# Performance work log

Measured on AMD Instinct MI355X. Metric: run time of the kernel, lower is better.

## Reference

```python
import jax, jax.numpy as jnp
import numpy as np

N_LAYER, D_MODEL, N_HEAD, D_HEAD, D_INNER = 4, 1024, 16, 64, 4096
QLEN, MLEN, BATCH, VOCAB = 512, 512, 4, 32000


def _layer_norm(x, g, b, eps=1e-5):
    mu = jnp.mean(x, axis=-1, keepdims=True)
    var = jnp.mean((x - mu) ** 2, axis=-1, keepdims=True)
    return (x - mu) * jax.lax.rsqrt(var + eps) * g + b


def _rel_shift(x):
    # x: [q, k, b, n] -- TransfoXL relative shift
    q, k, b, n = x.shape
    x = jnp.pad(x, ((0, 0), (1, 0), (0, 0), (0, 0)))
    return x.reshape(k + 1, q, b, n)[1:].reshape(q, k, b, n)


def _pos_emb(klen, d):
    inv_freq = 1.0 / (10000.0 ** (jnp.arange(0, d, 2, dtype=jnp.float32) / d))
    pos = jnp.arange(klen - 1, -1, -1, dtype=jnp.float32)
    sinusoid = pos[:, None] * inv_freq[None, :]
    return jnp.concatenate([jnp.sin(sinusoid), jnp.cos(sinusoid)], axis=-1)  # [klen, d]


def setup_inputs() -> dict:
    key = jax.random.key(0)
    ks = jax.random.split(key, 12)
    s = 0.02
    rn = lambda k, shape: jax.random.normal(k, shape, jnp.float32) * s
    return {
        "token_ids": jax.random.randint(ks[0], (BATCH, QLEN), 0, VOCAB),
        "mems": rn(ks[1], (N_LAYER, MLEN, BATCH, D_MODEL)),
        "word_emb": rn(ks[2], (VOCAB, D_MODEL)),
        "qkv_w": rn(ks[3], (N_LAYER, 3 * N_HEAD * D_HEAD, D_MODEL)),
        "o_w": rn(ks[4], (N_LAYER, D_MODEL, N_HEAD * D_HEAD)),
        "r_w": rn(ks[5], (N_LAYER, N_HEAD * D_HEAD, D_MODEL)),
        "r_w_bias": rn(ks[6], (N_LAYER, N_HEAD, D_HEAD)),
        "r_r_bias": rn(ks[7], (N_LAYER, N_HEAD, D_HEAD)),
        "ln1_g": jnp.ones((N_LAYER, D_MODEL)),
        "ln1_b": jnp.zeros((N_LAYER, D_MODEL)),
        "ff_w1": rn(ks[8], (N_LAYER, D_INNER, D_MODEL)),
        "ff_b1": jnp.zeros((N_LAYER, D_INNER)),
        "ff_w2": rn(ks[9], (N_LAYER, D_MODEL, D_INNER)),
        "ff_b2": jnp.zeros((N_LAYER, D_MODEL)),
        "ln2_g": jnp.ones((N_LAYER, D_MODEL)),
        "ln2_b": jnp.zeros((N_LAYER, D_MODEL)),
    }


def reference(token_ids, mems, word_emb, qkv_w, o_w, r_w, r_w_bias, r_r_bias,
              ln1_g, ln1_b, ff_w1, ff_b1, ff_w2, ff_b2, ln2_g, ln2_b):
    B, Q = token_ids.shape
    M = mems.shape[1]
    K = M + Q
    d_model = word_emb.shape[1]
    n_head, d_head = r_w_bias.shape[1], r_w_bias.shape[2]
    nd = n_head * d_head
    scale = 1.0 / (d_head ** 0.5)

    h = word_emb[token_ids].transpose(1, 0, 2)  # [Q, B, D] (TransfoXL is time-major)
    pe = _pos_emb(K, d_model)                   # [K, D]
    # causal mask: query i may attend keys j <= i + M
    mask = jnp.arange(K)[None, :] > (jnp.arange(Q)[:, None] + M)  # [Q, K]

    for l in range(mems.shape[0]):
        cat = jnp.concatenate([mems[l], h], axis=0)          # [K, B, D]
        qkv = jnp.einsum('kbd,ed->kbe', cat, qkv_w[l])       # [K, B, 3*nd]
        q = qkv[-Q:, :, :nd].reshape(Q, B, n_head, d_head)
        k = qkv[:, :, nd:2 * nd].reshape(K, B, n_head, d_head)
        v = qkv[:, :, 2 * nd:].reshape(K, B, n_head, d_head)
        r = (pe @ r_w[l].T).reshape(K, n_head, d_head)       # [K, n, d]

        AC = jnp.einsum('ibnd,jbnd->ijbn', q + r_w_bias[l], k)
        BD = _rel_shift(jnp.einsum('ibnd,jnd->ijbn', q + r_r_bias[l], r))
        score = (AC + BD) * scale                            # [Q, K, B, n]
        score = jnp.where(mask[:, :, None, None], -1e30, score)
        prob = jax.nn.softmax(score, axis=1)
        vec = jnp.einsum('ijbn,jbnd->ibnd', prob, v).reshape(Q, B, nd)
        h = _layer_norm(h + vec @ o_w[l].T, ln1_g[l], ln1_b[l])
        ff = jax.nn.relu(h @ ff_w1[l].T + ff_b1[l]) @ ff_w2[l].T + ff_b2[l]
        h = _layer_norm(h + ff, ln2_g[l], ln2_b[l])

    return h.transpose(1, 0, 2)  # [B, Q, D] last hidden state
```

## Files before the change

kernel.cpp:

```cpp
#include <hip/hip_runtime.h>
#include <cstdint>

#define NLAYER 4
#define DMODEL 1024
#define NHEAD 16
#define DHEAD 64
#define DINNER 4096
#define QLEN 512
#define MLEN 512
#define KLEN (QLEN + MLEN)
#define BATCH 4
#define ND (NHEAD * DHEAD)

typedef unsigned short u16;
typedef __attribute__((ext_vector_type(8))) short short8;
typedef __attribute__((ext_vector_type(4))) float f32x4;
typedef __attribute__((address_space(1))) const unsigned int guint;
typedef __attribute__((address_space(3))) unsigned int luint;

__device__ __forceinline__ u16 f2b(float x) {
  unsigned u = __builtin_bit_cast(unsigned, x);
  return (u16)((u + 0x7fffu + ((u >> 16) & 1u)) >> 16);
}
__device__ __forceinline__ float b2f(u16 h) {
  return __builtin_bit_cast(float, (unsigned)h << 16);
}

__global__ __launch_bounds__(256) void conv_bf16(
    const float* __restrict__ s, u16* __restrict__ d, int n8)
{
  const int i = blockIdx.x * 256 + threadIdx.x;
  if (i >= n8) return;
  const float4 a = ((const float4*)s)[2 * i], b = ((const float4*)s)[2 * i + 1];
  union { u16 u[8]; float4 v; } p;
  p.u[0] = f2b(a.x); p.u[1] = f2b(a.y); p.u[2] = f2b(a.z); p.u[3] = f2b(a.w);
  p.u[4] = f2b(b.x); p.u[5] = f2b(b.y); p.u[6] = f2b(b.z); p.u[7] = f2b(b.w);
  ((float4*)d)[i] = p.v;
}

__global__ __launch_bounds__(256) void embed_kernel(
    const int* __restrict__ tok, const float* __restrict__ emb,
    float* __restrict__ h, u16* __restrict__ hb)
{
  const int q = blockIdx.x, b = blockIdx.y, t = threadIdx.x;
  const int id = tok[b * QLEN + q];
  const float4 v = ((const float4*)(emb + (size_t)id * DMODEL))[t];
  const size_t row = (size_t)q * BATCH + b;
  ((float4*)(h + row * DMODEL))[t] = v;
  union { u16 u[4]; float2 f; } p;
  p.u[0] = f2b(v.x); p.u[1] = f2b(v.y); p.u[2] = f2b(v.z); p.u[3] = f2b(v.w);
  *(float2*)(hb + row * DMODEL + t * 4) = p.f;
}

__global__ __launch_bounds__(256) void posemb_kernel(u16* __restrict__ pe)
{
  const int k = blockIdx.x, t = threadIdx.x;
  const float pos = (float)(KLEN - 1 - k);
  for (int i = t; i < DMODEL / 2; i += 256) {
    const float inv_freq = powf(10000.0f, -(float)(2 * i) / (float)DMODEL);
    const float a = pos * inv_freq;
    pe[(size_t)k * DMODEL + i] = f2b(sinf(a));
    pe[(size_t)k * DMODEL + DMODEL / 2 + i] = f2b(cosf(a));
  }
}

template<int OUTBF, int RELU, int BIAS>
__global__ __launch_bounds__(256) void mgemm4(
    const u16* __restrict__ A0, const u16* __restrict__ A1, int splitRow,
    const u16* __restrict__ B, void* __restrict__ Cp,
    const float* __restrict__ bias, int Kd, long sa, long sb, long sc)
{
  constexpr int MF = 4;
  constexpr int BM = 128;
  constexpr int NGA = 16;
  constexpr int GPW = 8;
  __shared__ u16 As[2][BM][64];
  __shared__ u16 Bs[2][128][64];
  const int nwg = gridDim.x * gridDim.y;
  int wg = blockIdx.y * gridDim.x + blockIdx.x;
  wg = (wg & 7) * (nwg >> 3) + (wg >> 3);
  const int bm = (wg % gridDim.x) * BM;
  const int bn = (wg / gridDim.x) * 128;
  const int t = threadIdx.x, wave = t >> 6, lane = t & 63;
  const int wm = (wave >> 1) * (MF * 16), wn = (wave & 1) * 64;
  const int lrow = lane & 15, lk = lane >> 4;
  const int gsw = ((lane & 7) ^ (lane >> 3)) * 8;
  const u16* gptr[GPW];
  int row8[GPW];
  bool isA[GPW];
#pragma unroll
  for (int c = 0; c < GPW; ++c) {
    const int g = wave * GPW + c;
    isA[c] = g < NGA;
    row8[c] = (isA[c] ? g : g - NGA) * 8;
    const int row = row8[c] + (lane >> 3);
    if (isA[c]) {
      const int ga = bm + row;
      gptr[c] = ((A1 != nullptr && ga >= splitRow)
                     ? A1 + (size_t)(ga - splitRow) * sa
                     : A0 + (size_t)ga * sa) + gsw;
    } else {
      gptr[c] = B + (size_t)(bn + row) * sb + gsw;
    }
  }
  auto STAGE = [&](int buf, int k0) {
#pragma unroll
    for (int c = 0; c < GPW; ++c) {
      luint* dst = isA[c] ? (luint*)&As[buf][row8[c]][0] : (luint*)&Bs[buf][row8[c]][0];
      __builtin_amdgcn_global_load_lds((guint*)(gptr[c] + k0), dst, 16, 0, 0);
    }
  };
  f32x4 acc[MF][4] = {};
  const int nt = Kd >> 6;
  STAGE(0, 0);
  for (int ti = 0; ti < nt; ++ti) {
    const int cur = ti & 1;
    if (ti + 1 < nt) {
      STAGE(cur ^ 1, (ti + 1) << 6);
      asm volatile("s_waitcnt vmcnt(8)" ::: "memory");
    } else {
      asm volatile("s_waitcnt vmcnt(0)" ::: "memory");
    }
    __builtin_amdgcn_s_barrier();
    __builtin_amdgcn_sched_barrier(0);
    __builtin_amdgcn_s_setprio(1);
#pragma unroll
    for (int ks = 0; ks < 2; ++ks) {
      short8 af[MF], bf[4];
#pragma unroll
      for (int x = 0; x < MF; ++x) {
        const int ra = wm + x * 16 + lrow;
        af[x] = *(const short8*)((const u16*)&As[cur][0][0] + ra * 64 + (((ks * 4 + lk) ^ (ra & 7)) * 8));
      }
#pragma unroll
      for (int x = 0; x < 4; ++x) {
        const int rb = wn + x * 16 + lrow;
        bf[x] = *(const short8*)((const u16*)&Bs[cur][0][0] + rb * 64 + (((ks * 4 + lk) ^ (rb & 7)) * 8));
      }
#pragma unroll
      for (int mi = 0; mi < MF; ++mi)
#pragma unroll
        for (int ni = 0; ni < 4; ++ni)
          acc[mi][ni] = __builtin_amdgcn_mfma_f32_16x16x32_bf16(af[mi], bf[ni], acc[mi][ni], 0, 0, 0);
    }
    __builtin_amdgcn_s_setprio(0);
    asm volatile("s_waitcnt lgkmcnt(0)" ::: "memory");
    __builtin_amdgcn_s_barrier();
    __builtin_amdgcn_sched_barrier(0);
  }
  const size_t row0 = bm + wm + lk * 4;
  const size_t col0 = bn + wn + lrow;
#pragma unroll
  for (int mi = 0; mi < MF; ++mi)
#pragma unroll
    for (int r = 0; r < 4; ++r) {
      const size_t row = row0 + mi * 16 + r;
#pragma unroll
      for (int ni = 0; ni < 4; ++ni) {
        float v = acc[mi][ni][r];
        if (BIAS) v += bias[col0 + ni * 16];
        if (RELU) v = fmaxf(v, 0.0f);
        if (OUTBF) ((u16*)Cp)[row * sc + col0 + ni * 16] = f2b(v);
        else       ((float*)Cp)[row * sc + col0 + ni * 16] = v;
      }
    }
}

template<int BIAS>
__global__ __launch_bounds__(256) void mgemm4k(
    const u16* __restrict__ A, const u16* __restrict__ B,
    float* __restrict__ C0, float* __restrict__ C1,
    const float* __restrict__ bias, int KdH, long sa, long sb, long sc)
{
  constexpr int MF = 2;
  constexpr int BM = 64;
  constexpr int NGA = 8;
  constexpr int GPW = 6;
  __shared__ u16 As[2][BM][64];
  __shared__ u16 Bs[2][128][64];
  const int z = blockIdx.z;
  A += (size_t)z * KdH;
  B += (size_t)z * KdH;
  float* C = z ? C1 : C0;
  const int nwg = gridDim.x * gridDim.y;
  int wg = blockIdx.y * gridDim.x + blockIdx.x;
  wg = (wg & 7) * (nwg >> 3) + (wg >> 3);
  const int bm = (wg % gridDim.x) * BM;
  const int bn = (wg / gridDim.x) * 128;
  const int t = threadIdx.x, wave = t >> 6, lane = t & 63;
  const int wm = (wave >> 1) * (MF * 16), wn = (wave & 1) * 64;
  const int lrow = lane & 15, lk = lane >> 4;
  const int gsw = ((lane & 7) ^ (lane >> 3)) * 8;
  const u16* gptr[GPW];
  int row8[GPW];
  bool isA[GPW];
#pragma unroll
  for (int c = 0; c < GPW; ++c) {
    const int g = wave * GPW + c;
    isA[c] = g < NGA;
    row8[c] = (isA[c] ? g : g - NGA) * 8;
    const int row = row8[c] + (lane >> 3);
    gptr[c] = isA[c] ? A + (size_t)(bm + row) * sa + gsw
                     : B + (size_t)(bn + row) * sb + gsw;
  }
  auto STAGE = [&](int buf, int k0) {
#pragma unroll
    for (int c = 0; c < GPW; ++c) {
      luint* dst = isA[c] ? (luint*)&As[buf][row8[c]][0] : (luint*)&Bs[buf][row8[c]][0];
      __builtin_amdgcn_global_load_lds((guint*)(gptr[c] + k0), dst, 16, 0, 0);
    }
  };
  f32x4 acc[MF][4] = {};
  const int nt = KdH >> 6;
  STAGE(0, 0);
  for (int ti = 0; ti < nt; ++ti) {
    const int cur = ti & 1;
    if (ti + 1 < nt) {
      STAGE(cur ^ 1, (ti + 1) << 6);
      asm volatile("s_waitcnt vmcnt(6)" ::: "memory");
    } else {
      asm volatile("s_waitcnt vmcnt(0)" ::: "memory");
    }
    __builtin_amdgcn_s_barrier();
    __builtin_amdgcn_sched_barrier(0);
    __builtin_amdgcn_s_setprio(1);
#pragma unroll
    for (int ks = 0; ks < 2; ++ks) {
      short8 af[MF], bf[4];
#pragma unroll
      for (int x = 0; x < MF; ++x) {
        const int ra = wm + x * 16 + lrow;
        af[x] = *(const short8*)((const u16*)&As[cur][0][0] + ra * 64 + (((ks * 4 + lk) ^ (ra & 7)) * 8));
      }
#pragma unroll
      for (int x = 0; x < 4; ++x) {
        const int rb = wn + x * 16 + lrow;
        bf[x] = *(const short8*)((const u16*)&Bs[cur][0][0] + rb * 64 + (((ks * 4 + lk) ^ (rb & 7)) * 8));
      }
#pragma unroll
      for (int mi = 0; mi < MF; ++mi)
#pragma unroll
        for (int ni = 0; ni < 4; ++ni)
          acc[mi][ni] = __builtin_amdgcn_mfma_f32_16x16x32_bf16(af[mi], bf[ni], acc[mi][ni], 0, 0, 0);
    }
    __builtin_amdgcn_s_setprio(0);
    asm volatile("s_waitcnt lgkmcnt(0)" ::: "memory");
    __builtin_amdgcn_s_barrier();
    __builtin_amdgcn_sched_barrier(0);
  }
  const size_t row0 = bm + wm + lk * 4;
  const size_t col0 = bn + wn + lrow;
#pragma unroll
  for (int mi = 0; mi < MF; ++mi)
#pragma unroll
    for (int r = 0; r < 4; ++r) {
      const size_t row = row0 + mi * 16 + r;
#pragma unroll
      for (int ni = 0; ni < 4; ++ni) {
        float v = acc[mi][ni][r];
        if (BIAS && z == 0) v += bias[col0 + ni * 16];
        C[row * sc + col0 + ni * 16] = v;
      }
    }
}

template<int MF, int OUTBF, int RELU, int BIAS>
__global__ __launch_bounds__(256) void mgemm3(
    const u16* __restrict__ A0, const u16* __restrict__ A1, int splitRow,
    const u16* __restrict__ B, void* __restrict__ Cp,
    const float* __restrict__ bias, int Kd, long sa, long sb, long sc,
    long bzs, long czs)
{
  constexpr int BM = MF * 32;
  constexpr int NGA = BM / 8;
  constexpr int GPW = (NGA + 16) / 4;
  __shared__ u16 As[2][BM][64];
  __shared__ u16 Bs[2][128][64];
  const int zz = blockIdx.z;
  B += (size_t)zz * bzs;
  const int nwg = gridDim.x * gridDim.y;
  int wg = blockIdx.y * gridDim.x + blockIdx.x;
  wg = (wg & 7) * (nwg >> 3) + (wg >> 3);
  const int bm = (wg % gridDim.x) * BM;
  const int bn = (wg / gridDim.x) * 128;
  const int t = threadIdx.x, wave = t >> 6, lane = t & 63;
  const int wm = (wave >> 1) * (MF * 16), wn = (wave & 1) * 64;
  const int lrow = lane & 15, lk = lane >> 4;
  const int gsw = ((lane & 7) ^ (lane >> 3)) * 8;
  const u16* gptr[GPW];
  int row8[GPW];
  bool isA[GPW];
#pragma unroll
  for (int c = 0; c < GPW; ++c) {
    const int g = wave * GPW + c;
    isA[c] = g < NGA;
    row8[c] = (isA[c] ? g : g - NGA) * 8;
    const int row = row8[c] + (lane >> 3);
    if (isA[c]) {
      const int ga = bm + row;
      gptr[c] = ((A1 != nullptr && ga >= splitRow)
                     ? A1 + (size_t)(ga - splitRow) * sa
                     : A0 + (size_t)ga * sa) + gsw;
    } else {
      gptr[c] = B + (size_t)(bn + row) * sb + gsw;
    }
  }
  auto STAGE = [&](int buf, int k0) {
#pragma unroll
    for (int c = 0; c < GPW; ++c) {
      luint* dst = isA[c] ? (luint*)&As[buf][row8[c]][0] : (luint*)&Bs[buf][row8[c]][0];
      __builtin_amdgcn_global_load_lds((guint*)(gptr[c] + k0), dst, 16, 0, 0);
    }
  };
  f32x4 acc[MF][4] = {};
  const int nt = Kd >> 6;
  STAGE(0, 0);
  __syncthreads();
  for (int ti = 0; ti < nt; ++ti) {
    const int cur = ti & 1;
    if (ti + 1 < nt) STAGE(cur ^ 1, (ti + 1) << 6);
#pragma unroll
    for (int ks = 0; ks < 2; ++ks) {
      short8 af[MF], bf[4];
#pragma unroll
      for (int x = 0; x < MF; ++x) {
        const int ra = wm + x * 16 + lrow;
        af[x] = *(const short8*)((const u16*)&As[cur][0][0] + ra * 64 + (((ks * 4 + lk) ^ (ra & 7)) * 8));
      }
#pragma unroll
      for (int x = 0; x < 4; ++x) {
        const int rb = wn + x * 16 + lrow;
        bf[x] = *(const short8*)((const u16*)&Bs[cur][0][0] + rb * 64 + (((ks * 4 + lk) ^ (rb & 7)) * 8));
      }
#pragma unroll
      for (int mi = 0; mi < MF; ++mi)
#pragma unroll
        for (int ni = 0; ni < 4; ++ni)
          acc[mi][ni] = __builtin_amdgcn_mfma_f32_16x16x32_bf16(af[mi], bf[ni], acc[mi][ni], 0, 0, 0);
    }
    __syncthreads();
  }
  const size_t row0 = bm + wm + lk * 4;
  const size_t col0 = bn + wn + lrow;
#pragma unroll
  for (int mi = 0; mi < MF; ++mi)
#pragma unroll
    for (int r = 0; r < 4; ++r) {
      const size_t row = row0 + mi * 16 + r;
#pragma unroll
      for (int ni = 0; ni < 4; ++ni) {
        float v = acc[mi][ni][r];
        if (BIAS) v += bias[col0 + ni * 16];
        if (RELU) v = fmaxf(v, 0.0f);
        if (OUTBF) ((u16*)Cp + (size_t)zz * czs)[row * sc + col0 + ni * 16] = f2b(v);
        else       ((float*)Cp + (size_t)zz * czs)[row * sc + col0 + ni * 16] = v;
      }
    }
}

__global__ __launch_bounds__(256) void bd_gemm(
    const u16* __restrict__ qkvb, const u16* __restrict__ B,
    const float* __restrict__ rrb, u16* __restrict__ S)
{
  __shared__ u16 As[128][40];
  __shared__ u16 Bs[128][40];
  const int bm = blockIdx.x * 128, bn = blockIdx.y * 128;
  if (bm + bn < 257) return;
  const int z = blockIdx.z, zb = z & 3, zn = z >> 2;
  const u16* Ab = qkvb + ((size_t)(QLEN * BATCH) + zb) * (3 * ND) + zn * 64;
  const u16* Bb = B + zn * 64;
  u16* Sb = S + (size_t)(zn * 4 + zb) * 524288;
  const int t = threadIdx.x, wave = t >> 6, lane = t & 63;
  const int wm = (wave >> 1) * 64, wn = (wave & 1) * 64;
  const int lrow = lane & 15, lk = lane >> 4;
  const int srow = t >> 2, skc = (t & 3) * 8;
  f32x4 acc[4][4] = {};
  for (int k0 = 0; k0 < 64; k0 += 32) {
    union { u16 u[8]; float4 v; } a0, a1;
    a0.v = *(const float4*)(Ab + (size_t)(bm + srow) * (BATCH * 3 * ND) + k0 + skc);
    a1.v = *(const float4*)(Ab + (size_t)(bm + srow + 64) * (BATCH * 3 * ND) + k0 + skc);
#pragma unroll
    for (int e = 0; e < 8; ++e) {
      const float bias = rrb[zn * 64 + k0 + skc + e];
      a0.u[e] = f2b(b2f(a0.u[e]) + bias);
      a1.u[e] = f2b(b2f(a1.u[e]) + bias);
    }
    const float4 b0 = *(const float4*)(Bb + (size_t)(bn + srow) * 1024 + k0 + skc);
    const float4 b1 = *(const float4*)(Bb + (size_t)(bn + srow + 64) * 1024 + k0 + skc);
    __syncthreads();
    *(float4*)&As[srow][skc] = a0.v; *(float4*)&As[srow + 64][skc] = a1.v;
    *(float4*)&Bs[srow][skc] = b0;   *(float4*)&Bs[srow + 64][skc] = b1;
    __syncthreads();
    short8 af[4], bf[4];
#pragma unroll
    for (int x = 0; x < 4; ++x) af[x] = *(const short8*)&As[wm + x * 16 + lrow][lk * 8];
#pragma unroll
    for (int x = 0; x < 4; ++x) bf[x] = *(const short8*)&Bs[wn + x * 16 + lrow][lk * 8];
#pragma unroll
    for (int mi = 0; mi < 4; ++mi)
#pragma unroll
      for (int ni = 0; ni < 4; ++ni)
        acc[mi][ni] = __builtin_amdgcn_mfma_f32_16x16x32_bf16(af[mi], bf[ni], acc[mi][ni], 0, 0, 0);
  }
  const int row0 = bm + wm + lk * 4;
  const int col0 = bn + wn + lrow;
#pragma unroll
  for (int mi = 0; mi < 4; ++mi)
#pragma unroll
    for (int r = 0; r < 4; ++r) {
      const int row = row0 + mi * 16 + r;
#pragma unroll
      for (int ni = 0; ni < 4; ++ni) {
        const int j = col0 + ni * 16 + row - 511;
        if (j >= 0) Sb[(size_t)row * 1024 + j] = f2b(acc[mi][ni][r] * 0.125f);
      }
    }
}

__global__ __launch_bounds__(256) void vtrans_kernel(
    const u16* __restrict__ qkvb, u16* __restrict__ Vt)
{
  __shared__ u16 T[64][72];
  const int j0 = blockIdx.x * 64;
  const int bn = blockIdx.y, b = bn >> 4, n = bn & 15;
  const int t = threadIdx.x;
  const int jl = t >> 3, ch = t & 7;
#pragma unroll
  for (int p = 0; p < 2; ++p) {
    const int jj = p * 32 + jl;
    const float4 v = *(const float4*)(qkvb + ((size_t)(j0 + jj) * BATCH + b) * (3 * ND)
                                      + 2 * ND + n * 64 + ch * 8);
    *(float4*)&T[jj][ch * 8] = v;
  }
  __syncthreads();
#pragma unroll
  for (int p = 0; p < 2; ++p) {
    const int dd = p * 32 + jl;
    union { u16 u[8]; float4 v; } o;
#pragma unroll
    for (int e = 0; e < 8; ++e) o.u[e] = T[ch * 8 + e][dd];
    *(float4*)(Vt + ((size_t)(b * 16 + n) * 64 + dd) * 1024 + j0 + ch * 8) = o.v;
  }
}

__global__ __launch_bounds__(512) void flash_attn(
    const u16* __restrict__ qkvb, const u16* __restrict__ Vt,
    const u16* __restrict__ BDs, const float* __restrict__ rwb,
    u16* __restrict__ O)
{
  __shared__ u16 qs[128][72];
  __shared__ u16 ks[2][64][72];
  __shared__ u16 vs[2][64][72];
  __shared__ u16 ps[8][16][72];
  const int i0 = blockIdx.x * 128;
  const int n = blockIdx.y, b = blockIdx.z;
  const int t = threadIdx.x, wave = t >> 6, lane = t & 63;
  const int lrow = lane & 15, lk = lane >> 4;
  const int ilb = wave * 16 + lk * 4;
  {
    const int qr = t >> 2, qc = (t & 3) * 16;
    const u16* qsrc = qkvb + ((size_t)(QLEN + i0 + qr) * BATCH + b) * (3 * ND) + n * 64 + qc;
#pragma unroll
    for (int p = 0; p < 2; ++p) {
      union { u16 u[8]; float4 v; } q8;
      q8.v = *(const float4*)(qsrc + p * 8);
#pragma unroll
      for (int e = 0; e < 8; ++e)
        q8.u[e] = f2b((b2f(q8.u[e]) + rwb[n * 64 + qc + p * 8 + e]) * 0.125f);
      *(float4*)&qs[qr][qc + p * 8] = q8.v;
    }
  }
  const u16* bd = BDs + ((size_t)(n * 4 + b) * QLEN + i0) * 1024;
  const int ntiles = blockIdx.x * 2 + 10;
  const int jr = t >> 3, jc = (t & 7) * 8;

  float4 kr, vr;
  u16 bdn[16], bdc[16];
  auto LOADT = [&](int j0) {
    kr = *(const float4*)(qkvb + ((size_t)(j0 + jr) * BATCH + b) * (3 * ND) + ND + n * 64 + jc);
    vr = *(const float4*)(Vt + ((size_t)(b * 16 + n) * 64 + jr) * 1024 + j0 + jc);
#pragma unroll
    for (int nf = 0; nf < 4; ++nf)
#pragma unroll
      for (int r = 0; r < 4; ++r)
        bdn[nf * 4 + r] = bd[(size_t)(ilb + r) * 1024 + j0 + nf * 16 + lrow];
  };
  auto WRITET = [&](int buf) {
    *(float4*)&ks[buf][jr][jc] = kr;
    *(float4*)&vs[buf][jr][jc] = vr;
  };

  LOADT(0);
  WRITET(0);
#pragma unroll
  for (int e = 0; e < 16; ++e) bdc[e] = bdn[e];

  f32x4 o[4] = {};
  float m[4] = {-INFINITY, -INFINITY, -INFINITY, -INFINITY};
  float l[4] = {0.0f, 0.0f, 0.0f, 0.0f};

  for (int jt = 0; jt < ntiles; ++jt) {
    const int cur = jt & 1;
    const int j0 = jt * 64;
    __syncthreads();
    if (jt + 1 < ntiles) LOADT(j0 + 64);
    f32x4 s[4] = {};
    const short8 aq0 = *(const short8*)&qs[wave * 16 + lrow][lk * 8];
    const short8 aq1 = *(const short8*)&qs[wave * 16 + lrow][32 + lk * 8];
#pragma unroll
    for (int nf = 0; nf < 4; ++nf) {
      const short8 b0 = *(const short8*)&ks[cur][nf * 16 + lrow][lk * 8];
      const short8 b1 = *(const short8*)&ks[cur][nf * 16 + lrow][32 + lk * 8];
      s[nf] = __builtin_amdgcn_mfma_f32_16x16x32_bf16(aq0, b0, s[nf], 0, 0, 0);
      s[nf] = __builtin_amdgcn_mfma_f32_16x16x32_bf16(aq1, b1, s[nf], 0, 0, 0);
    }
    float sv[4][4];
#pragma unroll
    for (int nf = 0; nf < 4; ++nf)
#pragma unroll
      for (int r = 0; r < 4; ++r) {
        const int ig = i0 + ilb + r;
        const int jg = j0 + nf * 16 + lrow;
        const float val = s[nf][r] + b2f(bdc[nf * 4 + r]);
        sv[nf][r] = (jg <= ig + MLEN) ? val : -INFINITY;
      }
#pragma unroll
    for (int r = 0; r < 4; ++r) {
      float mt = fmaxf(fmaxf(sv[0][r], sv[1][r]), fmaxf(sv[2][r], sv[3][r]));
#pragma unroll
      for (int dx = 1; dx < 16; dx <<= 1) mt = fmaxf(mt, __shfl_xor(mt, dx));
      const float mnew = fmaxf(m[r], mt);
      const float alpha = __expf(m[r] - mnew);
      float ls = 0.0f;
#pragma unroll
      for (int nf = 0; nf < 4; ++nf) {
        const float pv = __expf(sv[nf][r] - mnew);
        sv[nf][r] = pv;
        ls += pv;
      }
#pragma unroll
      for (int dx = 1; dx < 16; dx <<= 1) ls += __shfl_xor(ls, dx);
      l[r] = l[r] * alpha + ls;
      m[r] = mnew;
#pragma unroll
      for (int nf = 0; nf < 4; ++nf) o[nf][r] *= alpha;
    }
#pragma unroll
    for (int nf = 0; nf < 4; ++nf)
#pragma unroll
      for (int r = 0; r < 4; ++r)
        ps[wave][lk * 4 + r][nf * 16 + lrow] = f2b(sv[nf][r]);
    asm volatile("s_waitcnt lgkmcnt(0)" ::: "memory");
    __builtin_amdgcn_sched_barrier(0);
    const short8 pa0 = *(const short8*)&ps[wave][lrow][lk * 8];
    const short8 pa1 = *(const short8*)&ps[wave][lrow][32 + lk * 8];
#pragma unroll
    for (int nf = 0; nf < 4; ++nf) {
      const short8 b0 = *(const short8*)&vs[cur][nf * 16 + lrow][lk * 8];
      const short8 b1 = *(const short8*)&vs[cur][nf * 16 + lrow][32 + lk * 8];
      o[nf] = __builtin_amdgcn_mfma_f32_16x16x32_bf16(pa0, b0, o[nf], 0, 0, 0);
      o[nf] = __builtin_amdgcn_mfma_f32_16x16x32_bf16(pa1, b1, o[nf], 0, 0, 0);
    }
    if (jt + 1 < ntiles) {
      WRITET(cur ^ 1);
#pragma unroll
      for (int e = 0; e < 16; ++e) bdc[e] = bdn[e];
    }
  }
#pragma unroll
  for (int r = 0; r < 4; ++r) {
    const float inv = 1.0f / l[r];
    const size_t ig = i0 + ilb + r;
#pragma unroll
    for (int nf = 0; nf < 4; ++nf)
      O[(ig * BATCH + b) * ND + n * 64 + nf * 16 + lrow] = f2b(o[nf][r] * inv);
  }
}

__global__ __launch_bounds__(256) void ln_residual_kernel(
    float* __restrict__ h, u16* __restrict__ hb,
    const float* __restrict__ d0, const float* __restrict__ d1,
    const float* __restrict__ g, const float* __restrict__ bb)
{
  const int row = blockIdx.x, t = threadIdx.x;
  __shared__ float xs[DMODEL];
  __shared__ float red[256];
  float s = 0.0f;
  for (int d = t; d < DMODEL; d += 256) {
    const size_t ix = (size_t)row * DMODEL + d;
    const float v = h[ix] + d0[ix] + d1[ix];
    xs[d] = v;
    s += v;
  }
  red[t] = s;
  __syncthreads();
  for (int w = 128; w > 0; w >>= 1) {
    if (t < w) red[t] += red[t + w];
    __syncthreads();
  }
  const float mean = red[0] * (1.0f / DMODEL);
  __syncthreads();
  float vs = 0.0f;
  for (int d = t; d < DMODEL; d += 256) {
    const float dv = xs[d] - mean;
    vs = fmaf(dv, dv, vs);
  }
  red[t] = vs;
  __syncthreads();
  for (int w = 128; w > 0; w >>= 1) {
    if (t < w) red[t] += red[t + w];
    __syncthreads();
  }
  const float rstd = rsqrtf(red[0] * (1.0f / DMODEL) + 1e-5f);
  for (int d = t; d < DMODEL; d += 256) {
    const float o = (xs[d] - mean) * rstd * g[d] + bb[d];
    h[(size_t)row * DMODEL + d] = o;
    hb[(size_t)row * DMODEL + d] = f2b(o);
  }
}

__global__ __launch_bounds__(256) void out_kernel(
    const float* __restrict__ h, float* __restrict__ out)
{
  const int q = blockIdx.x, b = blockIdx.y, t = threadIdx.x;
  const float4* src = (const float4*)(h + ((size_t)q * BATCH + b) * DMODEL);
  float4* dst = (float4*)(out + ((size_t)b * QLEN + q) * DMODEL);
  dst[t] = src[t];
}

extern "C" void kernel_launch(void* const* d_in, const int* in_sizes, int n_in,
                              void* d_out, int out_size, void* d_ws, size_t ws_size,
                              hipStream_t stream)
{
  const int*   tok  = (const int*)d_in[0];
  const float* mems = (const float*)d_in[1];
  const float* wemb = (const float*)d_in[2];
  const float* qkvw = (const float*)d_in[3];
  const float* ow   = (const float*)d_in[4];
  const float* rw   = (const float*)d_in[5];
  const float* rwb  = (const float*)d_in[6];
  const float* rrb  = (const float*)d_in[7];
  const float* ln1g = (const float*)d_in[8];
  const float* ln1b = (const float*)d_in[9];
  const float* ffw1 = (const float*)d_in[10];
  const float* ffb1 = (const float*)d_in[11];
  const float* ffw2 = (const float*)d_in[12];
  const float* ffb2 = (const float*)d_in[13];
  const float* ln2g = (const float*)d_in[14];
  const float* ln2b = (const float*)d_in[15];

  float* h      = (float*)d_ws;
  u16* S        = (u16*)(h + 2097152);
  float* tmp    = (float*)S;
  u16* h_bf     = S + 33554432;
  u16* qkv_bf   = h_bf + 2097152;
  u16* ffh_bf   = qkv_bf;
  u16* pe_bf    = qkv_bf + 12582912;
  u16* Vt       = pe_bf + 1048576;
  u16* vec_bf   = Vt + 4194304;
  u16* mems_bf  = vec_bf + 2097152;
  u16* wq = mems_bf + 8388608;
  u16* wo = wq + 12582912;
  u16* wr = wo + 4194304;
  u16* w1 = wr + 4194304;
  u16* w2 = w1 + 16777216;
  u16* rb_all = w2 + 16777216;
  float* tmp2 = (float*)(rb_all + 4194304);

  embed_kernel<<<dim3(QLEN, BATCH), 256, 0, stream>>>(tok, wemb, h, h_bf);
  posemb_kernel<<<KLEN, 256, 0, stream>>>(pe_bf);

#define CONV(src, dst, n) conv_bf16<<<(n) / 2048, 256, 0, stream>>>(src, dst, (n) / 8)
  CONV(mems, mems_bf, 8388608);
  CONV(qkvw, wq, 12582912);
  CONV(ow,   wo, 4194304);
  CONV(rw,   wr, 4194304);
  CONV(ffw1, w1, 16777216);
  CONV(ffw2, w2, 16777216);

  mgemm3<2, 1, 0, 0><<<dim3(16, 8, 4), 256, 0, stream>>>(
      pe_bf, nullptr, 0, wr, rb_all, nullptr,
      1024, 1024, 1024, 1024, 1048576, 1048576);

  for (int l = 0; l < NLAYER; ++l) {
    mgemm4<1, 0, 0><<<dim3(32, 24), 256, 0, stream>>>(
        mems_bf + (size_t)l * 2097152, h_bf, 2048,
        wq + (size_t)l * 3145728, qkv_bf, nullptr, 1024, 1024, 1024, 3072);

    vtrans_kernel<<<dim3(16, 64), 256, 0, stream>>>(qkv_bf, Vt);

    bd_gemm<<<dim3(4, 8, 64), 256, 0, stream>>>(
        qkv_bf, rb_all + (size_t)l * 1048576, rrb + (size_t)l * ND, S);

    flash_attn<<<dim3(4, 16, 4), 512, 0, stream>>>(
        qkv_bf, Vt, S, rwb + (size_t)l * ND, vec_bf);

    mgemm4k<0><<<dim3(32, 8, 2), 256, 0, stream>>>(
        vec_bf, wo + (size_t)l * 1048576, tmp, tmp2, nullptr,
        512, 1024, 1024, 1024);
    ln_residual_kernel<<<2048, 256, 0, stream>>>(
        h, h_bf, tmp, tmp2, ln1g + (size_t)l * DMODEL, ln1b + (size_t)l * DMODEL);
    mgemm4<1, 1, 1><<<dim3(16, 32), 256, 0, stream>>>(
        h_bf, nullptr, 0, w1 + (size_t)l * 4194304, ffh_bf,
        ffb1 + (size_t)l * DINNER, 1024, 1024, 1024, 4096);
    mgemm4k<1><<<dim3(32, 8, 2), 256, 0, stream>>>(
        ffh_bf, w2 + (size_t)l * 4194304, tmp, tmp2,
        ffb2 + (size_t)l * DMODEL, 2048, 4096, 4096, 1024);
    ln_residual_kernel<<<2048, 256, 0, stream>>>(
        h, h_bf, tmp, tmp2, ln2g + (size_t)l * DMODEL, ln2b + (size_t)l * DMODEL);
  }

  out_kernel<<<dim3(QLEN, BATCH), 256, 0, stream>>>(h, (float*)d_out);
}
```

Baseline: 875.1 us.

## Store split-K GEMM partials in bf16, vectorize LN residual, raise MFMA priority

The split-K GEMM (mgemm4k) now writes its two partial outputs as bf16 instead of fp32. The layernorm residual kernel reads them as bf16 and works on four elements per thread with vectorized loads and stores, keeping values in registers instead of shared memory. The attention kernel also raises wave priority around its MFMA blocks. Together these aim to cut memory traffic for the partials and LN, at the cost of extra rounding in the residual sums.

```diff
diff --git a/kernel.cpp b/kernel.cpp
--- a/kernel.cpp
+++ b/kernel.cpp
@@ -169,7 +169,7 @@
 template<int BIAS>
 __global__ __launch_bounds__(256) void mgemm4k(
     const u16* __restrict__ A, const u16* __restrict__ B,
-    float* __restrict__ C0, float* __restrict__ C1,
+    u16* __restrict__ C0, u16* __restrict__ C1,
     const float* __restrict__ bias, int KdH, long sa, long sb, long sc)
 {
   constexpr int MF = 2;
@@ -181,7 +181,7 @@
   const int z = blockIdx.z;
   A += (size_t)z * KdH;
   B += (size_t)z * KdH;
-  float* C = z ? C1 : C0;
+  u16* C = z ? C1 : C0;
   const int nwg = gridDim.x * gridDim.y;
   int wg = blockIdx.y * gridDim.x + blockIdx.x;
   wg = (wg & 7) * (nwg >> 3) + (wg >> 3);
@@ -259,7 +259,7 @@
       for (int ni = 0; ni < 4; ++ni) {
         float v = acc[mi][ni][r];
         if (BIAS && z == 0) v += bias[col0 + ni * 16];
-        C[row * sc + col0 + ni * 16] = v;
+        C[row * sc + col0 + ni * 16] = f2b(v);
       }
     }
 }
@@ -507,6 +507,7 @@
     f32x4 s[4] = {};
     const short8 aq0 = *(const short8*)&qs[wave * 16 + lrow][lk * 8];
     const short8 aq1 = *(const short8*)&qs[wave * 16 + lrow][32 + lk * 8];
+    __builtin_amdgcn_s_setprio(1);
 #pragma unroll
     for (int nf = 0; nf < 4; ++nf) {
       const short8 b0 = *(const short8*)&ks[cur][nf * 16 + lrow][lk * 8];
@@ -514,6 +515,7 @@
       s[nf] = __builtin_amdgcn_mfma_f32_16x16x32_bf16(aq0, b0, s[nf], 0, 0, 0);
       s[nf] = __builtin_amdgcn_mfma_f32_16x16x32_bf16(aq1, b1, s[nf], 0, 0, 0);
     }
+    __builtin_amdgcn_s_setprio(0);
     float sv[4][4];
 #pragma unroll
     for (int nf = 0; nf < 4; ++nf)
@@ -554,6 +556,7 @@
     __builtin_amdgcn_sched_barrier(0);
     const short8 pa0 = *(const short8*)&ps[wave][lrow][lk * 8];
     const short8 pa1 = *(const short8*)&ps[wave][lrow][32 + lk * 8];
+    __builtin_amdgcn_s_setprio(1);
 #pragma unroll
     for (int nf = 0; nf < 4; ++nf) {
       const short8 b0 = *(const short8*)&vs[cur][nf * 16 + lrow][lk * 8];
@@ -561,6 +564,7 @@
       o[nf] = __builtin_amdgcn_mfma_f32_16x16x32_bf16(pa0, b0, o[nf], 0, 0, 0);
       o[nf] = __builtin_amdgcn_mfma_f32_16x16x32_bf16(pa1, b1, o[nf], 0, 0, 0);
     }
+    __builtin_amdgcn_s_setprio(0);
     if (jt + 1 < ntiles) {
       WRITET(cur ^ 1);
 #pragma unroll
@@ -579,18 +583,22 @@
 
 __global__ __launch_bounds__(256) void ln_residual_kernel(
     float* __restrict__ h, u16* __restrict__ hb,
-    const float* __restrict__ d0, const float* __restrict__ d1,
+    const u16* __restrict__ d0, const u16* __restrict__ d1,
     const float* __restrict__ g, const float* __restrict__ bb)
 {
   const int row = blockIdx.x, t = threadIdx.x;
-  __shared__ float xs[DMODEL];
   __shared__ float red[256];
+  const size_t ix = (size_t)row * DMODEL + t * 4;
+  const float4 hv = *(const float4*)(h + ix);
+  union { u16 u[4]; float2 f; } a, b2;
+  a.f = *(const float2*)(d0 + ix);
+  b2.f = *(const float2*)(d1 + ix);
+  float x[4];
   float s = 0.0f;
-  for (int d = t; d < DMODEL; d += 256) {
-    const size_t ix = (size_t)row * DMODEL + d;
-    const float v = h[ix] + d0[ix] + d1[ix];
-    xs[d] = v;
-    s += v;
+#pragma unroll
+  for (int e = 0; e < 4; ++e) {
+    x[e] = ((const float*)&hv)[e] + b2f(a.u[e]) + b2f(b2.u[e]);
+    s += x[e];
   }
   red[t] = s;
   __syncthreads();
@@ -601,8 +609,9 @@
   const float mean = red[0] * (1.0f / DMODEL);
   __syncthreads();
   float vs = 0.0f;
-  for (int d = t; d < DMODEL; d += 256) {
-    const float dv = xs[d] - mean;
+#pragma unroll
+  for (int e = 0; e < 4; ++e) {
+    const float dv = x[e] - mean;
     vs = fmaf(dv, dv, vs);
   }
   red[t] = vs;
@@ -612,11 +621,18 @@
     __syncthreads();
   }
   const float rstd = rsqrtf(red[0] * (1.0f / DMODEL) + 1e-5f);
-  for (int d = t; d < DMODEL; d += 256) {
-    const float o = (xs[d] - mean) * rstd * g[d] + bb[d];
-    h[(size_t)row * DMODEL + d] = o;
-    hb[(size_t)row * DMODEL + d] = f2b(o);
-  }
+  const float4 gv = *(const float4*)(g + t * 4);
+  const float4 bv = *(const float4*)(bb + t * 4);
+  float4 ho;
+  union { u16 u[4]; float2 f; } po;
+#pragma unroll
+  for (int e = 0; e < 4; ++e) {
+    const float o = (x[e] - mean) * rstd * ((const float*)&gv)[e] + ((const float*)&bv)[e];
+    ((float*)&ho)[e] = o;
+    po.u[e] = f2b(o);
+  }
+  *(float4*)(h + ix) = ho;
+  *(float2*)(hb + ix) = po.f;
 }
 
 __global__ __launch_bounds__(256) void out_kernel(
@@ -651,7 +667,7 @@
 
   float* h      = (float*)d_ws;
   u16* S        = (u16*)(h + 2097152);
-  float* tmp    = (float*)S;
+  u16* tmp      = S;
   u16* h_bf     = S + 33554432;
   u16* qkv_bf   = h_bf + 2097152;
   u16* ffh_bf   = qkv_bf;
@@ -665,7 +681,7 @@
   u16* w1 = wr + 4194304;
   u16* w2 = w1 + 16777216;
   u16* rb_all = w2 + 16777216;
-  float* tmp2 = (float*)(rb_all + 4194304);
+  u16* tmp2 = rb_all + 4194304;
 
   embed_kernel<<<dim3(QLEN, BATCH), 256, 0, stream>>>(tok, wemb, h, h_bf);
   posemb_kernel<<<KLEN, 256, 0, stream>>>(pe_bf);
```

New measurement: 846.7 us. 3.2% less time.
